# Kernel optimization log

Hardware: AMD Instinct MI355X
Metric: run time of the kernel (lower is better)

## Reference

```python
import jax, jax.numpy as jnp
import numpy as np

N_HEADS = 16
ROPE_THETA = 10000.0


def _rope_cos_sin(T, head_dim, dtype):
    # freqs: (head_dim//2,), angles: (T, head_dim//2)
    freqs = 1.0 / ROPE_THETA ** (jnp.arange(0, head_dim, 2, dtype=jnp.float32) / head_dim)
    ang = jnp.arange(T, dtype=jnp.float32)[:, None] * freqs[None, :]
    return jnp.cos(ang).astype(dtype), jnp.sin(ang).astype(dtype)


def _apply_rope(x, cos, sin):
    # x: (B, H, T, D); cos/sin: (T, D//2)
    D = x.shape[-1]
    x1, x2 = x[..., : D // 2], x[..., D // 2 :]
    return jnp.concatenate([x1 * cos - x2 * sin, x1 * sin + x2 * cos], axis=-1)


def setup_inputs() -> dict:
    key = jax.random.key(0)
    ks = jax.random.split(key, 5)
    B, T, C = 2, 2048, 1024
    x = jax.random.normal(ks[0], (B, T, C), dtype=jnp.float32)
    w_attn = jax.random.normal(ks[1], (C, 3 * C), dtype=jnp.float32) * (C ** -0.5)
    b_attn = jax.random.normal(ks[2], (3 * C,), dtype=jnp.float32) * 0.02
    w_proj = jax.random.normal(ks[3], (C, C), dtype=jnp.float32) * (C ** -0.5)
    b_proj = jax.random.normal(ks[4], (C,), dtype=jnp.float32) * 0.02
    return {
        "x": x,
        "w_attn": w_attn,
        "b_attn": b_attn,
        "w_proj": w_proj,
        "b_proj": b_proj,
        "last_k_no_attend": 0,
        "window_size": 0,
    }


def reference(x, w_attn, b_attn, w_proj, b_proj, last_k_no_attend, window_size):
    B, T, C = x.shape
    H = N_HEADS
    D = C // H
    qkv = x @ w_attn + b_attn  # (B, T, 3C)
    q, k, v = jnp.split(qkv, 3, axis=-1)
    # (B, T, C) -> (B, H, T, D)
    to_heads = lambda t: t.reshape(B, T, H, D).transpose(0, 2, 1, 3)
    q, k, v = to_heads(q), to_heads(k), to_heads(v)
    cos, sin = _rope_cos_sin(T, D, x.dtype)
    q = _apply_rope(q, cos, sin)
    k = _apply_rope(k, cos, sin)
    scale = D ** -0.5
    attn = jnp.einsum("bhqd,bhkd->bhqk", q, k) * scale  # (B, H, T, T)
    causal = jnp.tril(jnp.ones((T, T), dtype=bool))
    attn = jnp.where(causal, attn, -jnp.inf)
    # last_k_no_attend/window_size default to 0 -> the custom-mask branch is
    # skipped (the nonzero branch in the source is ill-defined: it zeroes
    # entire rows producing NaN softmax).
    attn = jax.nn.softmax(attn, axis=-1)
    y = jnp.einsum("bhqk,bhkd->bhqd", attn, v)  # (B, H, T, D)
    y = y.transpose(0, 2, 1, 3).reshape(B, T, C)
    return y @ w_proj + b_proj
```

## Files before the change

kernel.cpp:

```cpp
#include <hip/hip_runtime.h>
#include <hip/hip_bf16.h>

typedef __bf16 bf16_t;
typedef __bf16 bf16x8 __attribute__((ext_vector_type(8)));
typedef float f32x4 __attribute__((ext_vector_type(4)));
typedef float f32x8v __attribute__((ext_vector_type(8)));

#define B_    2
#define T_    2048
#define C_    1024
#define H_    16
#define D_    64
#define M_    4096
#define NQKV_ 3072
#define PLD   72
#define NQT2  16
#define GTILE (128 * 64)

static __device__ __forceinline__ float  bf2f(bf16_t x) { return (float)x; }
static __device__ __forceinline__ bf16_t f2bf(float x)  { return (bf16_t)x; }

typedef const __attribute__((address_space(1))) void gas_void;
typedef __attribute__((address_space(3))) void las_void;
static __device__ __forceinline__ void gld16(const void* g, void* l) {
  __builtin_amdgcn_global_load_lds((gas_void*)g, (las_void*)l, 16, 0, 0);
}

__global__ __launch_bounds__(256) void rope_tab_k(float2* __restrict__ tab) {
  int i = blockIdx.x * 256 + threadIdx.x;
  int tpos = i >> 5, d = i & 31;
  float fr = exp2f(-(float)d * (13.287712379549449f / 32.0f));
  float ang = (float)tpos * fr;
  tab[i] = make_float2(cosf(ang), sinf(ang));
}

__global__ __launch_bounds__(256) void f32_to_bf16_k(const float* __restrict__ in,
                                                     bf16_t* __restrict__ out) {
  const int i = (blockIdx.x * 256 + threadIdx.x) * 8;
  f32x8v v = *(const f32x8v*)(in + i);
  bf16x8 h;
#pragma unroll
  for (int j = 0; j < 8; ++j) h[j] = f2bf(v[j]);
  *(bf16x8*)(out + i) = h;
}

__global__ __launch_bounds__(256) void transpose_f32_bf16(const float* __restrict__ in,
                                                          bf16_t* __restrict__ out,
                                                          int R, int Ccols) {
  __shared__ bf16_t tile[32][33];
  int tx = threadIdx.x & 31, ty = threadIdx.x >> 5;
  int c0 = blockIdx.x * 32, r0 = blockIdx.y * 32;
#pragma unroll
  for (int j = 0; j < 4; ++j)
    tile[ty + j * 8][tx] = f2bf(in[(size_t)(r0 + ty + j * 8) * Ccols + c0 + tx]);
  __syncthreads();
#pragma unroll
  for (int j = 0; j < 4; ++j)
    out[(size_t)(c0 + ty + j * 8) * R + r0 + tx] = tile[tx][ty + j * 8];
}

__device__ __forceinline__ void gemm_core(const bf16_t* __restrict__ A,
                                          const bf16_t* __restrict__ Bt,
                                          int m0, int n0,
                                          bf16_t* sm,
                                          f32x4 acc[4][4]) {
  const int t    = threadIdx.x;
  const int lane = t & 63, w = t >> 6;
  const int wr = (w >> 1) * 64, wc = (w & 1) * 64;
  const int l15 = lane & 15, g4 = lane >> 4;

  const f32x4 z4 = {0.f, 0.f, 0.f, 0.f};
#pragma unroll
  for (int i = 0; i < 4; ++i)
#pragma unroll
    for (int j = 0; j < 4; ++j) acc[i][j] = z4;

  const int srow = w * 32 + (lane >> 3);
  const int sel8 = (lane & 7) * 8;
  const bf16_t* gA = A  + (size_t)(m0 + srow) * C_ + sel8;
  const bf16_t* gB = Bt + (size_t)(n0 + srow) * C_ + sel8;
  const int dOff = (w * 32) * 64;

#pragma unroll
  for (int j = 0; j < 4; ++j) {
    gld16(gA + (size_t)(j * 8) * C_, sm + dOff + j * 8 * 64);
    gld16(gB + (size_t)(j * 8) * C_, sm + GTILE + dOff + j * 8 * 64);
  }
  __syncthreads();

  int cur = 0;
  for (int kt = 0; kt < C_ / 64; ++kt) {
    if (kt + 1 < C_ / 64) {
      const int k0 = (kt + 1) * 64;
      bf16_t* nA = sm + (cur ^ 1) * (2 * GTILE);
      bf16_t* nB = nA + GTILE;
#pragma unroll
      for (int j = 0; j < 4; ++j) {
        gld16(gA + (size_t)(j * 8) * C_ + k0, nA + dOff + j * 8 * 64);
        gld16(gB + (size_t)(j * 8) * C_ + k0, nB + dOff + j * 8 * 64);
      }
    }
    const bf16_t* lA = sm + cur * (2 * GTILE);
    const bf16_t* lB = lA + GTILE;
#pragma unroll
    for (int ks = 0; ks < 2; ++ks) {
      bf16x8 af[4], bfv[4];
#pragma unroll
      for (int mi = 0; mi < 4; ++mi)
        af[mi] = *(const bf16x8*)&lA[(wr + mi * 16 + l15) * 64 + ks * 32 + g4 * 8];
#pragma unroll
      for (int ni = 0; ni < 4; ++ni)
        bfv[ni] = *(const bf16x8*)&lB[(wc + ni * 16 + l15) * 64 + ks * 32 + g4 * 8];
#pragma unroll
      for (int mi = 0; mi < 4; ++mi)
#pragma unroll
        for (int ni = 0; ni < 4; ++ni)
          acc[mi][ni] = __builtin_amdgcn_mfma_f32_16x16x32_bf16(af[mi], bfv[ni],
                                                                acc[mi][ni], 0, 0, 0);
    }
    __syncthreads();
    cur ^= 1;
  }
}

__global__ __launch_bounds__(256) void qkv_gemm(const bf16_t* __restrict__ x,
                                                const bf16_t* __restrict__ wT,
                                                const float* __restrict__ bias,
                                                const float2* __restrict__ rtab,
                                                bf16_t* __restrict__ qo,
                                                bf16_t* __restrict__ ko,
                                                bf16_t* __restrict__ vo) {
  __shared__ __align__(16) bf16_t smem[4 * GTILE];
  f32x4 acc[4][4];
  const int bid = blockIdx.x;
  const int swz = (bid & 7) * 96 + (bid >> 3);
  const int m0 = (swz & 31) * 128, n0 = (swz >> 5) * 128;
  gemm_core(x, wT, m0, n0, smem, acc);

  const int t = threadIdx.x;
  const int lane = t & 63, w = t >> 6;
  const int wr = (w >> 1) * 64, wc = (w & 1) * 64;
  const int l15 = lane & 15, g4 = lane >> 4;
  const int ng  = n0 + wc;
  const int sel = ng >> 10;
  const int h   = (ng & 1023) >> 6;

  __syncthreads();
  bf16_t* stg = smem + w * (64 * 64);

  if (sel < 2) {
    const float qs = (sel == 0) ? 0.125f * 1.4426950408889634f : 1.0f;
#pragma unroll
    for (int mi = 0; mi < 4; ++mi) {
#pragma unroll
      for (int ni = 0; ni < 2; ++ni) {
        const int d1 = ni * 16 + l15;
        const float b1 = bias[ng + d1];
        const float b2 = bias[ng + d1 + 32];
#pragma unroll
        for (int r = 0; r < 4; ++r) {
          const int lrow = mi * 16 + g4 * 4 + r;
          const int tpos = (m0 + wr + lrow) & (T_ - 1);
          const float2 cs = rtab[tpos * 32 + d1];
          const float x1 = acc[mi][ni][r]     + b1;
          const float x2 = acc[mi][ni + 2][r] + b2;
          stg[lrow * 64 + d1]      = f2bf((x1 * cs.x - x2 * cs.y) * qs);
          stg[lrow * 64 + d1 + 32] = f2bf((x1 * cs.y + x2 * cs.x) * qs);
        }
      }
    }
  } else {
#pragma unroll
    for (int mi = 0; mi < 4; ++mi)
#pragma unroll
      for (int ni = 0; ni < 4; ++ni) {
        const int d = ni * 16 + l15;
        const float b1 = bias[ng + d];
#pragma unroll
        for (int r = 0; r < 4; ++r)
          stg[(mi * 16 + g4 * 4 + r) * 64 + d] = f2bf(acc[mi][ni][r] + b1);
      }
  }

  bf16_t* outp = (sel == 0) ? qo : (sel == 1 ? ko : vo);
  const int a  = lane >> 3;
  const int b8 = (lane & 7) * 8;
#pragma unroll
  for (int p = 0; p < 8; ++p) {
    const int lrow = p * 8 + a;
    const int row  = m0 + wr + lrow;
    const int tpos = row & (T_ - 1);
    const int bb   = row >> 11;
    uint4 val = *(const uint4*)&stg[lrow * 64 + b8];
    *(uint4*)(outp + ((size_t)(bb * H_ + h) * T_ + tpos) * D_ + b8) = val;
  }
}

__global__ __launch_bounds__(512) void attn_fwd(const bf16_t* __restrict__ q,
                                                const bf16_t* __restrict__ k,
                                                const bf16_t* __restrict__ v,
                                                bf16_t* __restrict__ y) {
  __shared__ __align__(16) bf16_t Ks[64 * 64];
  __shared__ __align__(16) bf16_t Vt[64 * PLD];
  const int t = threadIdx.x;
  const int lane = t & 63, w = t >> 6;
  const int l15 = lane & 15, g4 = lane >> 4;

  const int f   = blockIdx.x;
  const int idx = f & 255;
  const int bh  = idx & 31;
  const int p   = idx >> 5;
  const int qt  = (f >> 8) ? (15 - p) : p;
  const int qb  = qt * 128;
  const size_t hb = (size_t)bh * T_ * D_;

  const int qrow = qb + w * 16 + l15;
  bf16x8 qf[2];
  qf[0] = *(const bf16x8*)(q + hb + (size_t)qrow * D_ + g4 * 8);
  qf[1] = *(const bf16x8*)(q + hb + (size_t)qrow * D_ + 32 + g4 * 8);

  const f32x4 z4 = {0.f, 0.f, 0.f, 0.f};
  f32x4 o[4];
#pragma unroll
  for (int i = 0; i < 4; ++i) o[i] = z4;
  float mx = -1e30f, L = 0.f;

  const int skk = t >> 3;
  const int sd0 = (t & 7) * 8;
  const int u   = t & 7;
  const int ksw = sd0 ^ ((skk & 7) * 8);
  const int slot = ((skk >> 5) & 1) * 32 + ((skk >> 2) & 3) * 8 + ((skk >> 4) & 1) * 4 + (skk & 3);
  const int pos  = (((slot >> 3) ^ u) << 3) | (slot & 7);
  const int rowb = qb + w * 16 + g4 * 4;

  const int ntiles = 2 * qt + 2;

  uint4 kv = *(const uint4*)(k + hb + (size_t)skk * D_ + sd0);
  uint4 vv = *(const uint4*)(v + hb + (size_t)skk * D_ + sd0);

  for (int it = 0; it < ntiles; ++it) {
    const int kb = it * 64;
    __syncthreads();
    *(uint4*)&Ks[skk * 64 + ksw] = kv;
    {
      const bf16_t* vb = (const bf16_t*)&vv;
#pragma unroll
      for (int i = 0; i < 8; ++i)
        Vt[(sd0 + i) * PLD + pos] = vb[i];
    }
    __syncthreads();

    if (it + 1 < ntiles) {
      const size_t nb = hb + (size_t)(kb + 64 + skk) * D_ + sd0;
      kv = *(const uint4*)(k + nb);
      vv = *(const uint4*)(v + nb);
    }

    const bool last = (it == ntiles - 1);
    if (last && w < 4) continue;

    f32x4 s[4];
#pragma unroll
    for (int c = 0; c < 4; ++c) s[c] = z4;
#pragma unroll
    for (int ks = 0; ks < 2; ++ks)
#pragma unroll
      for (int c = 0; c < 4; ++c) {
        const int kr = c * 16 + l15;
        bf16x8 kf = *(const bf16x8*)&Ks[kr * 64 + ((ks * 32 + g4 * 8) ^ ((kr & 7) * 8))];
        s[c] = __builtin_amdgcn_mfma_f32_16x16x32_bf16(kf, qf[ks], s[c], 0, 0, 0);
      }

    if (last || (it == ntiles - 2 && w < 4)) {
#pragma unroll
      for (int c = 0; c < 4; ++c)
#pragma unroll
        for (int r = 0; r < 4; ++r)
          if (kb + c * 16 + g4 * 4 + r > qrow) s[c][r] = -1e30f;
    }

    float tm = -1e30f;
#pragma unroll
    for (int c = 0; c < 4; ++c)
#pragma unroll
      for (int r = 0; r < 4; ++r) tm = fmaxf(tm, s[c][r]);
    tm = fmaxf(tm, __shfl_xor(tm, 16));
    tm = fmaxf(tm, __shfl_xor(tm, 32));
    if (!__all(tm - mx <= 8.0f)) {
      const float mnew = fmaxf(mx, tm);
      const float sc = exp2f(mx - mnew);
      L *= sc;
      float scr[4];
#pragma unroll
      for (int r = 0; r < 4; ++r)
        scr[r] = __shfl(sc, (lane & 48) | (g4 * 4 + r));
#pragma unroll
      for (int nf = 0; nf < 4; ++nf)
#pragma unroll
        for (int r = 0; r < 4; ++r) o[nf][r] *= scr[r];
      mx = mnew;
    }
    float rs = 0.f;
#pragma unroll
    for (int c = 0; c < 4; ++c)
#pragma unroll
      for (int r = 0; r < 4; ++r) {
        s[c][r] = exp2f(s[c][r] - mx);
        rs += s[c][r];
      }
    rs += __shfl_xor(rs, 16);
    rs += __shfl_xor(rs, 32);
    L += rs;

    bf16x8 ap0, ap1;
#pragma unroll
    for (int r = 0; r < 4; ++r) {
      ap0[r]     = f2bf(s[0][r]);
      ap0[4 + r] = f2bf(s[1][r]);
      ap1[r]     = f2bf(s[2][r]);
      ap1[4 + r] = f2bf(s[3][r]);
    }

#pragma unroll
    for (int nf = 0; nf < 4; ++nf) {
      const int d  = nf * 16 + l15;
      const int h3 = (2 * nf + (l15 >> 3)) & 7;
      bf16x8 vf0 = *(const bf16x8*)&Vt[d * PLD + ((g4 ^ h3) << 3)];
      bf16x8 vf1 = *(const bf16x8*)&Vt[d * PLD + (((g4 + 4) ^ h3) << 3)];
      o[nf] = __builtin_amdgcn_mfma_f32_16x16x32_bf16(ap0, vf0, o[nf], 0, 0, 0);
      o[nf] = __builtin_amdgcn_mfma_f32_16x16x32_bf16(ap1, vf1, o[nf], 0, 0, 0);
    }
  }

  const int bb = bh / H_, hh = bh % H_;
  float il[4];
#pragma unroll
  for (int r = 0; r < 4; ++r)
    il[r] = 1.0f / __shfl(L, (lane & 48) | (g4 * 4 + r));
#pragma unroll
  for (int nf = 0; nf < 4; ++nf)
#pragma unroll
    for (int r = 0; r < 4; ++r) {
      const int row = rowb + r;
      y[(size_t)(bb * T_ + row) * C_ + hh * D_ + nf * 16 + l15] = f2bf(o[nf][r] * il[r]);
    }
}

__global__ __launch_bounds__(256) void proj_gemm(const bf16_t* __restrict__ yin,
                                                 const bf16_t* __restrict__ wT,
                                                 const float* __restrict__ bias,
                                                 float* __restrict__ out) {
  __shared__ __align__(16) bf16_t smem[4 * GTILE];
  f32x4 acc[4][4];
  const int bid = blockIdx.x;
  const int swz = (bid & 7) * 32 + (bid >> 3);
  const int m0 = (swz & 31) * 128, n0 = (swz >> 5) * 128;
  gemm_core(yin, wT, m0, n0, smem, acc);

  const int t = threadIdx.x;
  const int lane = t & 63, w = t >> 6;
  const int wr = (w >> 1) * 64, wc = (w & 1) * 64;
  const int l15 = lane & 15, g4 = lane >> 4;
  const int ng = n0 + wc;
#pragma unroll
  for (int mi = 0; mi < 4; ++mi) {
    const int rowb = m0 + wr + mi * 16 + g4 * 4;
#pragma unroll
    for (int ni = 0; ni < 4; ++ni) {
      const int n = ng + ni * 16 + l15;
      const float b1 = bias[n];
#pragma unroll
      for (int r = 0; r < 4; ++r)
        out[(size_t)(rowb + r) * C_ + n] = acc[mi][ni][r] + b1;
    }
  }
}

extern "C" void kernel_launch(void* const* d_in, const int* in_sizes, int n_in,
                              void* d_out, int out_size, void* d_ws, size_t ws_size,
                              hipStream_t stream) {
  (void)in_sizes; (void)n_in; (void)out_size; (void)ws_size;
  const float* x      = (const float*)d_in[0];
  const float* w_attn = (const float*)d_in[1];
  const float* b_attn = (const float*)d_in[2];
  const float* w_proj = (const float*)d_in[3];
  const float* b_proj = (const float*)d_in[4];
  float* out = (float*)d_out;

  char* ws = (char*)d_ws;
  bf16_t* wTa = (bf16_t*)ws;  ws += (size_t)NQKV_ * C_ * 2;
  bf16_t* wTp = (bf16_t*)ws;  ws += (size_t)C_ * C_ * 2;
  bf16_t* qb  = (bf16_t*)ws;  ws += (size_t)B_ * H_ * T_ * D_ * 2;
  bf16_t* kb  = (bf16_t*)ws;  ws += (size_t)B_ * H_ * T_ * D_ * 2;
  bf16_t* vb  = (bf16_t*)ws;  ws += (size_t)B_ * H_ * T_ * D_ * 2;
  bf16_t* yb  = (bf16_t*)ws;  ws += (size_t)B_ * T_ * C_ * 2;
  float2* rtab = (float2*)ws; ws += (size_t)T_ * 32 * sizeof(float2);
  bf16_t* x_bf = yb;

  rope_tab_k<<<dim3(T_ * 32 / 256), 256, 0, stream>>>(rtab);
  transpose_f32_bf16<<<dim3(NQKV_ / 32, C_ / 32), 256, 0, stream>>>(w_attn, wTa, C_, NQKV_);
  transpose_f32_bf16<<<dim3(C_ / 32,   C_ / 32), 256, 0, stream>>>(w_proj, wTp, C_, C_);
  f32_to_bf16_k<<<dim3(M_ * C_ / (256 * 8)), 256, 0, stream>>>(x, x_bf);
  qkv_gemm<<<dim3((M_ / 128) * (NQKV_ / 128)), 256, 0, stream>>>(x_bf, wTa, b_attn, rtab, qb, kb, vb);
  attn_fwd<<<dim3(NQT2 * 32), 512, 0, stream>>>(qb, kb, vb, yb);
  proj_gemm<<<dim3((M_ / 128) * (C_ / 128)), 256, 0, stream>>>(yb, wTp, b_proj, out);
}
```

Baseline: 123.3 us.

## Enlarge QKV GEMM tiles to 256x256 with a four-stage async LDS ring

Rewrites the QKV projection GEMM so each block uses 512 threads and computes a 256x256 output tile instead of 128x128. The K loop takes steps of 32 through a four-slot ring buffer filled by global_load_lds, waiting on vmcnt and hitting one barrier per step. The aim is more operand reuse per LDS load and fewer barriers per MFMA. In exchange the grid shrinks to 192 blocks, which may leave CUs idle. Each wave now holds 128 accumulator registers, and the unswizzled 64-byte LDS rows may cause bank conflicts.

```diff
diff --git a/kernel.cpp b/kernel.cpp
--- a/kernel.cpp
+++ b/kernel.cpp
@@ -16,6 +16,7 @@
 #define PLD   72
 #define NQT2  16
 #define GTILE (128 * 64)
+#define SLOTE 16384
 
 static __device__ __forceinline__ float  bf2f(bf16_t x) { return (float)x; }
 static __device__ __forceinline__ bf16_t f2bf(float x)  { return (bf16_t)x; }
@@ -123,35 +124,84 @@
   }
 }
 
-__global__ __launch_bounds__(256) void qkv_gemm(const bf16_t* __restrict__ x,
-                                                const bf16_t* __restrict__ wT,
-                                                const float* __restrict__ bias,
-                                                const float2* __restrict__ rtab,
-                                                bf16_t* __restrict__ qo,
-                                                bf16_t* __restrict__ ko,
-                                                bf16_t* __restrict__ vo) {
-  __shared__ __align__(16) bf16_t smem[4 * GTILE];
-  f32x4 acc[4][4];
-  const int bid = blockIdx.x;
-  const int swz = (bid & 7) * 96 + (bid >> 3);
-  const int m0 = (swz & 31) * 128, n0 = (swz >> 5) * 128;
-  gemm_core(x, wT, m0, n0, smem, acc);
-
+__global__ __launch_bounds__(512, 2) void qkv_gemm(const bf16_t* __restrict__ x,
+                                                   const bf16_t* __restrict__ wT,
+                                                   const float* __restrict__ bias,
+                                                   const float2* __restrict__ rtab,
+                                                   bf16_t* __restrict__ qo,
+                                                   bf16_t* __restrict__ ko,
+                                                   bf16_t* __restrict__ vo) {
+  __shared__ __align__(16) bf16_t sm[4 * SLOTE];
   const int t = threadIdx.x;
   const int lane = t & 63, w = t >> 6;
-  const int wr = (w >> 1) * 64, wc = (w & 1) * 64;
   const int l15 = lane & 15, g4 = lane >> 4;
+  const int wr = (w >> 2) * 128, wc = (w & 3) * 64;
+
+  const int bid = blockIdx.x;
+  const int swz = (bid & 7) * 24 + (bid >> 3);
+  const int m0 = (swz & 15) * 256, n0 = (swz >> 4) * 256;
+
+  const f32x4 z4 = {0.f, 0.f, 0.f, 0.f};
+  f32x4 acc[8][4];
+#pragma unroll
+  for (int i = 0; i < 8; ++i)
+#pragma unroll
+    for (int j = 0; j < 4; ++j) acc[i][j] = z4;
+
+  const int sr  = (lane >> 2);
+  const int sc8 = (lane & 3) * 8;
+  const bf16_t* gA = x  + (size_t)(m0 + w * 32 + sr) * C_ + sc8;
+  const bf16_t* gB = wT + (size_t)(n0 + w * 32 + sr) * C_ + sc8;
+
+#define QKV_STAGE(h)                                                            \
+  {                                                                             \
+    bf16_t* sl = sm + ((h) & 3) * SLOTE;                                        \
+    const size_t kofs = (size_t)(h) * 32;                                       \
+    gld16(gA + kofs,            sl + (w * 32) * 32);                            \
+    gld16(gA + 16 * C_ + kofs,  sl + (w * 32 + 16) * 32);                       \
+    gld16(gB + kofs,            sl + 8192 + (w * 32) * 32);                     \
+    gld16(gB + 16 * C_ + kofs,  sl + 8192 + (w * 32 + 16) * 32);                \
+  }
+
+  QKV_STAGE(0);
+  QKV_STAGE(1);
+
+  for (int h = 0; h < 32; ++h) {
+    if (h < 31) asm volatile("s_waitcnt vmcnt(4)" ::: "memory");
+    else        asm volatile("s_waitcnt vmcnt(0)" ::: "memory");
+    __builtin_amdgcn_sched_barrier(0);
+    __builtin_amdgcn_s_barrier();
+    __builtin_amdgcn_sched_barrier(0);
+    if (h + 2 < 32) QKV_STAGE(h + 2);
+
+    const bf16_t* sl = sm + (h & 3) * SLOTE;
+    bf16x8 af[8], bfv[4];
+#pragma unroll
+    for (int mi = 0; mi < 8; ++mi)
+      af[mi] = *(const bf16x8*)&sl[(wr + mi * 16 + l15) * 32 + g4 * 8];
+#pragma unroll
+    for (int ni = 0; ni < 4; ++ni)
+      bfv[ni] = *(const bf16x8*)&sl[8192 + (wc + ni * 16 + l15) * 32 + g4 * 8];
+#pragma unroll
+    for (int mi = 0; mi < 8; ++mi)
+#pragma unroll
+      for (int ni = 0; ni < 4; ++ni)
+        acc[mi][ni] = __builtin_amdgcn_mfma_f32_16x16x32_bf16(af[mi], bfv[ni],
+                                                              acc[mi][ni], 0, 0, 0);
+  }
+#undef QKV_STAGE
+
+  __syncthreads();
+  bf16_t* stg = sm + w * 8192;
+
   const int ng  = n0 + wc;
   const int sel = ng >> 10;
-  const int h   = (ng & 1023) >> 6;
-
-  __syncthreads();
-  bf16_t* stg = smem + w * (64 * 64);
+  const int h2  = (ng & 1023) >> 6;
 
   if (sel < 2) {
     const float qs = (sel == 0) ? 0.125f * 1.4426950408889634f : 1.0f;
 #pragma unroll
-    for (int mi = 0; mi < 4; ++mi) {
+    for (int mi = 0; mi < 8; ++mi) {
 #pragma unroll
       for (int ni = 0; ni < 2; ++ni) {
         const int d1 = ni * 16 + l15;
@@ -171,7 +221,7 @@
     }
   } else {
 #pragma unroll
-    for (int mi = 0; mi < 4; ++mi)
+    for (int mi = 0; mi < 8; ++mi)
 #pragma unroll
       for (int ni = 0; ni < 4; ++ni) {
         const int d = ni * 16 + l15;
@@ -186,13 +236,13 @@
   const int a  = lane >> 3;
   const int b8 = (lane & 7) * 8;
 #pragma unroll
-  for (int p = 0; p < 8; ++p) {
+  for (int p = 0; p < 16; ++p) {
     const int lrow = p * 8 + a;
     const int row  = m0 + wr + lrow;
     const int tpos = row & (T_ - 1);
     const int bb   = row >> 11;
     uint4 val = *(const uint4*)&stg[lrow * 64 + b8];
-    *(uint4*)(outp + ((size_t)(bb * H_ + h) * T_ + tpos) * D_ + b8) = val;
+    *(uint4*)(outp + ((size_t)(bb * H_ + h2) * T_ + tpos) * D_ + b8) = val;
   }
 }
 
@@ -401,7 +451,7 @@
   transpose_f32_bf16<<<dim3(NQKV_ / 32, C_ / 32), 256, 0, stream>>>(w_attn, wTa, C_, NQKV_);
   transpose_f32_bf16<<<dim3(C_ / 32,   C_ / 32), 256, 0, stream>>>(w_proj, wTp, C_, C_);
   f32_to_bf16_k<<<dim3(M_ * C_ / (256 * 8)), 256, 0, stream>>>(x, x_bf);
-  qkv_gemm<<<dim3((M_ / 128) * (NQKV_ / 128)), 256, 0, stream>>>(x_bf, wTa, b_attn, rtab, qb, kb, vb);
+  qkv_gemm<<<dim3((M_ / 256) * (NQKV_ / 256)), 512, 0, stream>>>(x_bf, wTa, b_attn, rtab, qb, kb, vb);
   attn_fwd<<<dim3(NQT2 * 32), 512, 0, stream>>>(qb, kb, vb, yb);
   proj_gemm<<<dim3((M_ / 128) * (C_ / 128)), 256, 0, stream>>>(yb, wTp, b_proj, out);
 }
```

New measurement: 118.3 us. 1.04x faster.
